# Kernel optimization log

Hardware: AMD Instinct MI355X
Metric: run time of the kernel (lower is better)

Reference implementation:

```python
import jax, jax.numpy as jnp
import numpy as np

B, D, K = 4096, 2048, 8
RANGE_MIN, RANGE_MAX = -5.0, 5.0
MIN_BIN, MIN_SLOPE, MAX_SLOPE = 1e-3, 1e-3, 10.0


def setup_inputs() -> dict:
    key = jax.random.key(0)
    kx, kp = jax.random.split(key)
    x = jax.random.normal(kx, (B, D), dtype=jnp.float32)
    params = jax.random.normal(kp, (D, 3 * K + 1), dtype=jnp.float32) * 0.01
    return {"x": x, "params": params}


def _normalize_params(params):
    # params: [D, 3K+1] -> x_knots [D,K+1], y_knots [D,K+1], slopes [D,K+1]
    widths_raw = params[:, :K]
    heights_raw = params[:, K:2 * K]
    slopes_raw = params[:, 2 * K:]
    total_range = RANGE_MAX - RANGE_MIN
    remaining = total_range - K * MIN_BIN
    ws = jax.nn.sigmoid(widths_raw)
    widths = MIN_BIN + ws * remaining / jnp.sum(ws, axis=-1, keepdims=True)
    hs = jax.nn.sigmoid(heights_raw)
    heights = MIN_BIN + hs * remaining / jnp.sum(hs, axis=-1, keepdims=True)
    slopes = MIN_SLOPE + jax.nn.sigmoid(slopes_raw) * (MAX_SLOPE - MIN_SLOPE)
    pad = jnp.full((params.shape[0], 1), RANGE_MIN, dtype=params.dtype)
    x_knots = jnp.concatenate([pad, RANGE_MIN + jnp.cumsum(widths, axis=-1)], axis=-1)
    y_knots = jnp.concatenate([pad, RANGE_MIN + jnp.cumsum(heights, axis=-1)], axis=-1)
    return x_knots, y_knots, slopes


def reference(x, params):
    # x: [B, D]; params: [D, 3K+1] -> (y [B,D], total_logdet [B])
    x_knots, y_knots, slopes = _normalize_params(params)
    d_idx = jnp.arange(params.shape[0])[None, :]  # [1, D]

    below = x <= RANGE_MIN
    above = x >= RANGE_MAX
    s0 = slopes[:, 0][None, :]   # [1, D]
    sK = slopes[:, -1][None, :]  # [1, D]
    y_below = RANGE_MIN + (x - RANGE_MIN) * s0
    y_above = RANGE_MAX + (x - RANGE_MAX) * sK

    # searchsorted(x_knots[1:-1], x, side='right') == count of interior knots <= x
    bin_idx = jnp.sum(x_knots[None, :, 1:-1] <= x[:, :, None], axis=-1)  # [B, D]
    bin_idx = jnp.clip(bin_idx, 0, K - 1)

    x_k = x_knots[d_idx, bin_idx]
    x_k1 = x_knots[d_idx, bin_idx + 1]
    y_k = y_knots[d_idx, bin_idx]
    y_k1 = y_knots[d_idx, bin_idx + 1]
    d_k = slopes[d_idx, bin_idx]
    d_k1 = slopes[d_idx, bin_idx + 1]

    width = x_k1 - x_k
    height = y_k1 - y_k
    xi = (x - x_k) / width
    s = height / width
    xi1 = 1.0 - xi
    numerator = s * xi * xi + d_k * xi * xi1
    denominator = s + (d_k1 + d_k - 2.0 * s) * xi * xi1
    y_spline = y_k + height * numerator / denominator
    deriv_num = s * s * (d_k1 * xi * xi + 2.0 * s * xi * xi1 + d_k * xi1 * xi1)
    derivative = deriv_num / (denominator * denominator)

    y = jnp.where(below, y_below, jnp.where(above, y_above, y_spline))
    logdet = jnp.where(below, jnp.log(s0),
                       jnp.where(above, jnp.log(sK), jnp.log(derivative)))
    return y, jnp.sum(logdet, axis=-1)
```

## Files before the change

kernel.cpp:

```cpp
#include <hip/hip_runtime.h>
#include <hip/hip_bf16.h>

#define KBINS 8
#define DDIM 2048
#define BROWS 4096
#define NPAR 25
#define RPB 16
#define RCHUNK 8

__device__ __forceinline__ float fast_rcp(float a) {
    return __builtin_amdgcn_rcpf(a);
}

__device__ __forceinline__ float fsigmoid(float t) {
    return fast_rcp(1.0f + __expf(-t));
}

__global__ __launch_bounds__(128) void normalize_kernel(
        const float* __restrict__ params, float* __restrict__ tab) {
    const int d = blockIdx.x * 128 + (int)threadIdx.x;
    const float RMIN = -5.0f, RMAX = 5.0f;
    const float MIN_BIN = 1e-3f, MIN_SLOPE = 1e-3f, MAX_SLOPE = 10.0f;
    const float remaining = (RMAX - RMIN) - KBINS * MIN_BIN;

    const float* p = params + d * NPAR;
    float pr[NPAR];
#pragma unroll
    for (int i = 0; i < NPAR; ++i) pr[i] = p[i];

    float ws[KBINS], hs[KBINS];
    float wsum = 0.0f, hsum = 0.0f;
#pragma unroll
    for (int k = 0; k < KBINS; ++k) { ws[k] = fsigmoid(pr[k]); wsum += ws[k]; }
#pragma unroll
    for (int k = 0; k < KBINS; ++k) { hs[k] = fsigmoid(pr[KBINS + k]); hsum += hs[k]; }

    const float wscale = remaining * fast_rcp(wsum);
    const float hscale = remaining * fast_rcp(hsum);

#pragma unroll
    for (int k = 0; k <= KBINS; ++k)
        tab[k * DDIM + d] = MIN_SLOPE + (MAX_SLOPE - MIN_SLOPE) * fsigmoid(pr[2 * KBINS + k]);

    float cx = RMIN, cy = RMIN;
#pragma unroll
    for (int k = 0; k < KBINS; ++k) {
        cx += MIN_BIN + ws[k] * wscale;
        cy += MIN_BIN + hs[k] * hscale;
        tab[(9 + k) * DDIM + d] = cx;
        tab[(17 + k) * DDIM + d] = cy;
    }
}

__global__ __launch_bounds__(256, 6) void rqs_kernel(
        const float* __restrict__ x_in, const float* __restrict__ tab,
        float* __restrict__ y_out, float* __restrict__ logdet) {
    __shared__ float lt[25 * 256];

    const int tid = (int)threadIdx.x;
    const int c0 = (blockIdx.x & 7) * 256;
    const int d = c0 + tid;
    const int b0 = (int)(blockIdx.x >> 3) * RPB;

    const float RMIN = -5.0f, RMAX = 5.0f;

#pragma unroll
    for (int r = 0; r < 25; ++r) lt[r * 256 + tid] = tab[r * DDIM + c0 + tid];
    __syncthreads();

    float xkr[7];
#pragma unroll
    for (int j = 0; j < 7; ++j) xkr[j] = lt[(9 + j) * 256 + tid];
    const float s0 = lt[0 * 256 + tid];
    const float sK = lt[8 * 256 + tid];
    const float log_s0 = __logf(s0), log_sK = __logf(sK);

    const float* ltp = lt + tid;

    for (int rc = 0; rc < RPB; rc += RCHUNK) {
        float xv[RCHUNK];
#pragma unroll
        for (int r = 0; r < RCHUNK; ++r)
            xv[r] = x_in[(size_t)(b0 + rc + r) * DDIM + d];

        float ldv[RCHUNK];
#pragma unroll
        for (int r = 0; r < RCHUNK; ++r) {
            const float x = xv[r];
            int bin = 0;
#pragma unroll
            for (int j = 0; j < 7; ++j) bin += (xkr[j] <= x) ? 1 : 0;

            const float* base = ltp + bin * 256;
            const float dk   = base[0];
            const float dk1  = base[256];
            float x_k        = base[8 * 256];
            const float x_k1 = base[9 * 256];
            float y_k        = base[16 * 256];
            const float y_k1 = base[17 * 256];
            const bool bz = (bin == 0);
            x_k = bz ? RMIN : x_k;
            y_k = bz ? RMIN : y_k;

            const float w = x_k1 - x_k;
            const float h = y_k1 - y_k;
            const float inv_w = fast_rcp(w);
            const float xi  = (x - x_k) * inv_w;
            const float s   = h * inv_w;
            const float xi1 = 1.0f - xi;
            const float xx  = xi * xi1;
            const float xi2 = xi * xi;

            const float num = fmaf(s, xi2, dk * xx);
            const float den = fmaf(fmaf(-2.0f, s, dk1 + dk), xx, s);
            const float inv_den = fast_rcp(den);

            const float y_sp = fmaf(h * num, inv_den, y_k);
            const float inner = fmaf(dk1, xi2, fmaf(s + s, xx, dk * (xi1 * xi1)));
            const float t = s * inv_den;

            const bool below = x <= RMIN;
            const bool above = x >= RMAX;
            float y  = below ? fmaf(x - RMIN, s0, RMIN)
                     : above ? fmaf(x - RMAX, sK, RMAX) : y_sp;
            float ld = below ? log_s0
                     : above ? log_sK : __logf(t * t * inner);

            y_out[(size_t)(b0 + rc + r) * DDIM + d] = y;
            ldv[r] = ld;
        }

#pragma unroll
        for (int off = 32; off > 0; off >>= 1) {
#pragma unroll
            for (int r = 0; r < RCHUNK; ++r)
                ldv[r] += __shfl_down(ldv[r], off);
        }
        if ((tid & 63) == 0) {
#pragma unroll
            for (int r = 0; r < RCHUNK; ++r)
                atomicAdd(&logdet[b0 + rc + r], ldv[r]);
        }
    }
}

extern "C" void kernel_launch(void* const* d_in, const int* in_sizes, int n_in,
                              void* d_out, int out_size, void* d_ws, size_t ws_size,
                              hipStream_t stream) {
    const float* x = (const float*)d_in[0];
    const float* params = (const float*)d_in[1];
    float* out = (float*)d_out;
    float* y_out = out;
    float* logdet = out + (size_t)BROWS * DDIM;
    float* tab = (float*)d_ws;

    hipMemsetAsync(logdet, 0, BROWS * sizeof(float), stream);

    normalize_kernel<<<DDIM / 128, 128, 0, stream>>>(params, tab);

    const int grid = 8 * (BROWS / RPB);
    rqs_kernel<<<grid, 256, 0, stream>>>(x, tab, y_out, logdet);
}
```

Measured before the change: 120.6 us.

## Keep spline tables in registers, prefetch x, and use DPP wave reduction

Drops the 25KB shared-memory table and the syncthreads. Each thread now loads its column's knots and slopes into registers and picks the bin with a branchless select chain instead of indexed LDS reads. It also software-pipelines the x loads by prefetching the next chunk of 4 rows, replaces the shuffle-based wave reduction with DPP row ops, and raises the occupancy hint to 8. Register pressure grows from holding 26 table values per thread, and the select chain adds ALU work per element.

```diff
diff --git a/kernel.cpp b/kernel.cpp
--- a/kernel.cpp
+++ b/kernel.cpp
@@ -6,7 +6,8 @@
 #define BROWS 4096
 #define NPAR 25
 #define RPB 16
-#define RCHUNK 8
+#define RCHUNK 4
+#define NCHUNK (RPB / RCHUNK)
 
 __device__ __forceinline__ float fast_rcp(float a) {
     return __builtin_amdgcn_rcpf(a);
@@ -14,6 +15,22 @@
 
 __device__ __forceinline__ float fsigmoid(float t) {
     return fast_rcp(1.0f + __expf(-t));
+}
+
+template<int CTRL, int ROWMASK>
+__device__ __forceinline__ float dpp_add(float v) {
+    int r = __builtin_amdgcn_update_dpp(0, __float_as_int(v), CTRL, ROWMASK, 0xf, false);
+    return v + __int_as_float(r);
+}
+
+__device__ __forceinline__ float wave_sum64(float v) {
+    v = dpp_add<0x111, 0xf>(v);
+    v = dpp_add<0x112, 0xf>(v);
+    v = dpp_add<0x114, 0xf>(v);
+    v = dpp_add<0x118, 0xf>(v);
+    v = dpp_add<0x142, 0xa>(v);
+    v = dpp_add<0x143, 0xc>(v);
+    return v;
 }
 
 __global__ __launch_bounds__(128) void normalize_kernel(
@@ -52,55 +69,57 @@
     }
 }
 
-__global__ __launch_bounds__(256, 6) void rqs_kernel(
+__global__ __launch_bounds__(256, 8) void rqs_kernel(
         const float* __restrict__ x_in, const float* __restrict__ tab,
         float* __restrict__ y_out, float* __restrict__ logdet) {
-    __shared__ float lt[25 * 256];
-
     const int tid = (int)threadIdx.x;
-    const int c0 = (blockIdx.x & 7) * 256;
-    const int d = c0 + tid;
+    const int d = (blockIdx.x & 7) * 256 + tid;
     const int b0 = (int)(blockIdx.x >> 3) * RPB;
 
     const float RMIN = -5.0f, RMAX = 5.0f;
 
+    float sl[9], xk[9], yk[9];
 #pragma unroll
-    for (int r = 0; r < 25; ++r) lt[r * 256 + tid] = tab[r * DDIM + c0 + tid];
-    __syncthreads();
+    for (int k = 0; k < 9; ++k) sl[k] = tab[k * DDIM + d];
+#pragma unroll
+    for (int k = 1; k < 9; ++k) xk[k] = tab[(8 + k) * DDIM + d];
+#pragma unroll
+    for (int k = 1; k < 9; ++k) yk[k] = tab[(16 + k) * DDIM + d];
 
-    float xkr[7];
+    const float log_s0 = __logf(sl[0]);
+    const float log_sK = __logf(sl[8]);
+
+    float xv[RCHUNK], xn[RCHUNK];
 #pragma unroll
-    for (int j = 0; j < 7; ++j) xkr[j] = lt[(9 + j) * 256 + tid];
-    const float s0 = lt[0 * 256 + tid];
-    const float sK = lt[8 * 256 + tid];
-    const float log_s0 = __logf(s0), log_sK = __logf(sK);
+    for (int r = 0; r < RCHUNK; ++r)
+        xv[r] = x_in[(size_t)(b0 + r) * DDIM + d];
 
-    const float* ltp = lt + tid;
-
-    for (int rc = 0; rc < RPB; rc += RCHUNK) {
-        float xv[RCHUNK];
+#pragma unroll 1
+    for (int rc = 0; rc < NCHUNK; ++rc) {
+        if (rc + 1 < NCHUNK) {
 #pragma unroll
-        for (int r = 0; r < RCHUNK; ++r)
-            xv[r] = x_in[(size_t)(b0 + rc + r) * DDIM + d];
+            for (int r = 0; r < RCHUNK; ++r)
+                xn[r] = x_in[(size_t)(b0 + (rc + 1) * RCHUNK + r) * DDIM + d];
+        }
 
         float ldv[RCHUNK];
 #pragma unroll
         for (int r = 0; r < RCHUNK; ++r) {
             const float x = xv[r];
-            int bin = 0;
+
+            float x_k = RMIN, x_k1 = xk[1];
+            float y_k = RMIN, y_k1 = yk[1];
+            float dk = sl[0], dk1 = sl[1];
 #pragma unroll
-            for (int j = 0; j < 7; ++j) bin += (xkr[j] <= x) ? 1 : 0;
-
-            const float* base = ltp + bin * 256;
-            const float dk   = base[0];
-            const float dk1  = base[256];
-            float x_k        = base[8 * 256];
-            const float x_k1 = base[9 * 256];
-            float y_k        = base[16 * 256];
-            const float y_k1 = base[17 * 256];
-            const bool bz = (bin == 0);
-            x_k = bz ? RMIN : x_k;
-            y_k = bz ? RMIN : y_k;
+            for (int j = 1; j < 8; ++j) {
+                const bool c = xk[j] <= x;
+                x_k  = c ? xk[j]     : x_k;
+                x_k1 = c ? xk[j + 1] : x_k1;
+                y_k  = c ? yk[j]     : y_k;
+                y_k1 = c ? yk[j + 1] : y_k1;
+                dk   = c ? sl[j]     : dk;
+                dk1  = c ? sl[j + 1] : dk1;
+            }
 
             const float w = x_k1 - x_k;
             const float h = y_k1 - y_k;
@@ -121,26 +140,25 @@
 
             const bool below = x <= RMIN;
             const bool above = x >= RMAX;
-            float y  = below ? fmaf(x - RMIN, s0, RMIN)
-                     : above ? fmaf(x - RMAX, sK, RMAX) : y_sp;
+            float y  = below ? fmaf(x - RMIN, sl[0], RMIN)
+                     : above ? fmaf(x - RMAX, sl[8], RMAX) : y_sp;
             float ld = below ? log_s0
                      : above ? log_sK : __logf(t * t * inner);
 
-            y_out[(size_t)(b0 + rc + r) * DDIM + d] = y;
+            y_out[(size_t)(b0 + rc * RCHUNK + r) * DDIM + d] = y;
             ldv[r] = ld;
         }
 
 #pragma unroll
-        for (int off = 32; off > 0; off >>= 1) {
+        for (int r = 0; r < RCHUNK; ++r) ldv[r] = wave_sum64(ldv[r]);
+        if ((tid & 63) == 63) {
 #pragma unroll
             for (int r = 0; r < RCHUNK; ++r)
-                ldv[r] += __shfl_down(ldv[r], off);
+                atomicAdd(&logdet[b0 + rc * RCHUNK + r], ldv[r]);
         }
-        if ((tid & 63) == 0) {
+
 #pragma unroll
-            for (int r = 0; r < RCHUNK; ++r)
-                atomicAdd(&logdet[b0 + rc + r], ldv[r]);
-        }
+        for (int r = 0; r < RCHUNK; ++r) xv[r] = xn[r];
     }
 }
 
```

Measured after the change: 118.3 us. About the same (-1.9%).
